# Kernel tuning notes

Measured on AMD Instinct MI355X. Metric: run time of the kernel, lower is better.

The kernel has to match this reference:

```python
import jax, jax.numpy as jnp
import numpy as np

H, P, N, D, T, MLPW, B = 64, 4, 16, 8, 64, 512, 2048
D_IN = 1 + H + P * H  # 321


def _linear_init(key, i, o):
    k1, k2 = jax.random.split(key)
    s = 1.0 / np.sqrt(i)
    W = jax.random.uniform(k1, (i, o), jnp.float32, -s, s)
    b = jax.random.uniform(k2, (o,), jnp.float32, -s, s)
    return W, b


def setup_inputs() -> dict:
    key = jax.random.key(0)
    ks = jax.random.split(key, 10)
    dims_f = [(D_IN, MLPW), (MLPW, MLPW), (MLPW, MLPW), (MLPW, H)]
    dims_g = [(D_IN, MLPW), (MLPW, MLPW), (MLPW, MLPW), (MLPW, H * N)]
    inp = {}
    for idx, (i, o) in enumerate(dims_f):
        W, b = _linear_init(ks[idx], i, o)
        inp[f"fW{idx}"], inp[f"fb{idx}"] = W, b
    for idx, (i, o) in enumerate(dims_g):
        W, b = _linear_init(ks[4 + idx], i, o)
        inp[f"gW{idx}"], inp[f"gb{idx}"] = W, b
    inp["rW"], inp["rb"] = _linear_init(ks[8], H, D)
    inp["ts"] = jnp.arange(T, dtype=jnp.float32)  # uniform grid, dt = 1
    inp["dbt"] = jax.random.normal(ks[9], (T - 1, B, N), jnp.float32)  # per-step randn noise
    inp["batch_size"] = B
    return inp


def _mlp(x, params):
    # Linear+ReLU stack, final Linear with tanh (tscale=1.0)
    for W, b in params[:-1]:
        x = jax.nn.relu(x @ W + b)
    W, b = params[-1]
    return jnp.tanh(x @ W + b)


def _forward(ts, dbt, fp, gp, rW, rb, batch_size):
    x0 = jnp.ones((batch_size, H), jnp.float32)  # fixed=True initial state
    dt = ts[1] - ts[0]  # dt_scale = 1
    hist = jnp.zeros((T, batch_size, H), jnp.float32).at[0].set(x0)
    curr_x, curr_t = x0, ts[0]
    xs = [x0]
    for k in range(T - 1):  # one integration step per output interval (uniform ts)
        # ortho rfft over the growing state history (length k+1); keep first P coeffs,
        # real part (matches torch complex -> .float() cast), zero-pad to P.
        coeffs = jnp.fft.rfft(hist[: k + 1], axis=0, norm="ortho")  # (F, B, H) complex
        c = jnp.real(coeffs[:P]).astype(jnp.float32)
        if c.shape[0] < P:
            c = jnp.concatenate(
                [c, jnp.zeros((P - c.shape[0], batch_size, H), jnp.float32)], axis=0
            )
        feats = jnp.transpose(c, (1, 0, 2)).reshape(batch_size, P * H)  # (B, P*H)
        tcol = jnp.broadcast_to(jnp.reshape(curr_t, (1, 1)), (batch_size, 1))
        tx = jnp.concatenate([tcol, curr_x, feats], axis=1)  # (B, 1+H+P*H)
        drift = _mlp(tx, fp)  # (B, H)
        diff = _mlp(tx, gp).reshape(batch_size, H, N)  # (B, H, N)
        curr_x = curr_x + drift * dt + jnp.einsum("bhn,bn->bh", diff, dbt[k])
        curr_t = jnp.minimum(curr_t + dt, ts[-1])
        hist = hist.at[k + 1].set(curr_x)
        xs.append(curr_x)  # linear_interp degenerates to curr_x on uniform grid
    xs = jnp.stack(xs, axis=1)  # (B, T, H)
    ys = xs @ rW + rb  # readout, (B, T, D)
    tse = jnp.broadcast_to(ts[None, :, None], (batch_size, T, 1))
    # linear_interpolation_coeffs is identity for NaN-free data
    return jnp.concatenate([tse, ys], axis=2)  # (B, T, 1+D)


def reference(fW0, fb0, fW1, fb1, fW2, fb2, fW3, fb3,
              gW0, gb0, gW1, gb1, gW2, gb2, gW3, gb3,
              rW, rb, ts, dbt, batch_size):
    fp = [(fW0, fb0), (fW1, fb1), (fW2, fb2), (fW3, fb3)]
    gp = [(gW0, gb0), (gW1, gb1), (gW2, gb2), (gW3, gb3)]
    return _forward(ts, dbt, fp, gp, rW, rb, batch_size)
```

## Files before the change

### kernel.cpp

```cpp
#include <hip/hip_runtime.h>
#include <math.h>

constexpr int kH   = 64;
constexpr int kP   = 4;
constexpr int kN   = 16;
constexpr int kD   = 8;
constexpr int kT   = 64;
constexpr int kWd  = 512;
constexpr int kB   = 2048;
constexpr int kDIN = 1 + kH + kP * kH;
constexpr int kKP  = 384;
constexpr int kBH  = kB * kH;

typedef __attribute__((ext_vector_type(8))) short short8;
typedef __attribute__((ext_vector_type(4))) float f32x4;
typedef __attribute__((ext_vector_type(4))) float float4v;

__device__ __forceinline__ short f2bf(float x) {
    union { float f; unsigned u; } v; v.f = x;
    unsigned r = (v.u + 0x7FFFu + ((v.u >> 16) & 1u)) >> 16;
    return (short)r;
}

__device__ __forceinline__ void gload16(const short* g, short* l) {
    __builtin_amdgcn_global_load_lds(
        (const __attribute__((address_space(1))) unsigned int*)g,
        (__attribute__((address_space(3))) unsigned int*)l, 16, 0, 0);
}

__global__ __launch_bounds__(256) void transpose_bf16(const float* __restrict__ W,
                                                      short* __restrict__ Wt,
                                                      int K, int N, int Kp, int Np) {
    int idx = blockIdx.x * 256 + threadIdx.x;
    if (idx >= Kp * Np) return;
    int n = idx / Kp, kk = idx % Kp;
    float v = (kk < K && n < N) ? W[(size_t)kk * N + n] : 0.f;
    Wt[idx] = f2bf(v);
}

__global__ __launch_bounds__(256) void prep_bias(const float* __restrict__ fb0,
                                                 const float* __restrict__ gb0,
                                                 float* __restrict__ b0c) {
    int i = blockIdx.x * 256 + threadIdx.x;
    if (i < 1024) b0c[i] = (i < kWd) ? fb0[i] : gb0[i - kWd];
}

__global__ __launch_bounds__(256) void init_k(float* __restrict__ hist,
                                              short* __restrict__ txh) {
    int idx = blockIdx.x * 256 + threadIdx.x;
    if (idx < kBH) hist[idx] = 1.0f;
    if (idx < kB * (kKP - kDIN)) {
        int b = idx / (kKP - kDIN), c = idx % (kKP - kDIN);
        txh[(size_t)b * kKP + kDIN + c] = 0;
    }
}

__global__ __launch_bounds__(256) void step_pre(float* __restrict__ hist,
                                                const float* __restrict__ drift,
                                                const float* __restrict__ xdelta,
                                                short* __restrict__ txh, int k) {
    const int L = k + 1;
    __shared__ float ctab[kT * kP];
    int tid = threadIdx.x;
    float invs = rsqrtf((float)L);
    for (int i = tid; i < L * kP; i += 256) {
        int j = i >> 2, p = i & 3;
        ctab[i] = cosf(6.283185307179586f * (float)(p * j) / (float)L) * invs;
    }
    __syncthreads();
    int idx = blockIdx.x * 256 + tid;
    int b = idx >> 6, h = idx & 63;
    float xk;
    if (k == 0) {
        xk = 1.0f;
    } else {
        xk = hist[(size_t)(k - 1) * kBH + idx] + drift[idx] + xdelta[idx];
        hist[(size_t)k * kBH + idx] = xk;
    }
    const float* hp = hist + (size_t)b * kH + h;
    float a0 = 0.f, a1 = 0.f, a2 = 0.f, a3 = 0.f;
    for (int j = 0; j < k; ++j) {
        float x = hp[(size_t)j * kBH];
        a0 += x * ctab[j * 4 + 0];
        a1 += x * ctab[j * 4 + 1];
        a2 += x * ctab[j * 4 + 2];
        a3 += x * ctab[j * 4 + 3];
    }
    a0 += xk * ctab[k * 4 + 0];
    a1 += xk * ctab[k * 4 + 1];
    a2 += xk * ctab[k * 4 + 2];
    a3 += xk * ctab[k * 4 + 3];
    if (L < 2) a1 = 0.f;
    if (L < 4) a2 = 0.f;
    if (L < 6) a3 = 0.f;
    short* th = txh + (size_t)b * kKP;
    th[1 + kH + 0 * kH + h] = f2bf(a0);
    th[1 + kH + 1 * kH + h] = f2bf(a1);
    th[1 + kH + 2 * kH + h] = f2bf(a2);
    th[1 + kH + 3 * kH + h] = f2bf(a3);
    th[1 + h] = f2bf(xk);
    if (h == 0) th[0] = f2bf((float)k);
}

struct MArg {
    const short* A;
    const short* Bt;
    const float* bias;
    short* Cb;
    int K, lda, ldc, Nw;
};

__global__ __launch_bounds__(512, 1) void gemm128(MArg f, MArg g, int ysplit) {
    const int y = blockIdx.y;
    MArg a;
    int n0;
    if (y < ysplit) { a = f; n0 = y * 64; }
    else            { a = g; n0 = (y - ysplit) * 64; }
    const int m0 = blockIdx.x * 128;

    __shared__ __align__(16) short sA[2][2][128 * 32];
    __shared__ __align__(16) short sB[2][2][64 * 32];

    const int tid = threadIdx.x;
    const int lane = tid & 63;
    const int w = tid >> 6;
    const int wm = (w & 3) * 32;
    const int wn = (w >> 2) * 32;

    const int sr = tid >> 2;
    const int s  = tid & 3;
    const int scol = (s ^ ((sr >> 1) & 3)) * 8;
    const int sdst = sr * 32 + s * 8;
    const bool doB = tid < 256;

    const short* gA = a.A  + (size_t)(m0 + sr) * a.lda + scol;
    const short* gB = a.Bt + (size_t)(n0 + sr) * a.K   + scol;

    const int nk = a.K >> 6;
    f32x4 acc[2][2] = {};

    gload16(gA,      &sA[0][0][sdst]);
    gload16(gA + 32, &sA[0][1][sdst]);
    if (doB) {
        gload16(gB,      &sB[0][0][sdst]);
        gload16(gB + 32, &sB[0][1][sdst]);
    }

    const int fr = lane & 15;
    const int kb = ((lane >> 4) ^ ((fr >> 1) & 3)) * 8;
    const int ra0 = (wm + fr) * 32 + kb, ra1 = (wm + 16 + fr) * 32 + kb;
    const int rb0 = (wn + fr) * 32 + kb, rb1 = (wn + 16 + fr) * 32 + kb;

    for (int kt = 0; kt < nk; ++kt) {
        __syncthreads();
        const int cur = kt & 1, nxt = cur ^ 1;
        if (kt + 1 < nk) {
            const int ko = (kt + 1) << 6;
            gload16(gA + ko,      &sA[nxt][0][sdst]);
            gload16(gA + ko + 32, &sA[nxt][1][sdst]);
            if (doB) {
                gload16(gB + ko,      &sB[nxt][0][sdst]);
                gload16(gB + ko + 32, &sB[nxt][1][sdst]);
            }
        }
#pragma unroll
        for (int ks = 0; ks < 2; ++ks) {
            short8 a0 = *(const short8*)&sA[cur][ks][ra0];
            short8 a1 = *(const short8*)&sA[cur][ks][ra1];
            short8 b0 = *(const short8*)&sB[cur][ks][rb0];
            short8 b1 = *(const short8*)&sB[cur][ks][rb1];
            acc[0][0] = __builtin_amdgcn_mfma_f32_16x16x32_bf16(a0, b0, acc[0][0], 0, 0, 0);
            acc[0][1] = __builtin_amdgcn_mfma_f32_16x16x32_bf16(a0, b1, acc[0][1], 0, 0, 0);
            acc[1][0] = __builtin_amdgcn_mfma_f32_16x16x32_bf16(a1, b0, acc[1][0], 0, 0, 0);
            acc[1][1] = __builtin_amdgcn_mfma_f32_16x16x32_bf16(a1, b1, acc[1][1], 0, 0, 0);
        }
    }

    const int rq = (lane >> 4) * 4;
#pragma unroll
    for (int jj = 0; jj < 2; ++jj) {
        int n = n0 + wn + jj * 16 + fr;
        if (n >= a.Nw) continue;
        float bv = a.bias[n];
#pragma unroll
        for (int i = 0; i < 2; ++i)
#pragma unroll
            for (int r = 0; r < 4; ++r) {
                int m = m0 + wm + i * 16 + rq + r;
                a.Cb[(size_t)m * a.ldc + n] = f2bf(fmaxf(acc[i][jj][r] + bv, 0.f));
            }
    }
}

__global__ __launch_bounds__(512, 1) void l4_kernel(const short* __restrict__ b1,
                                                    const short* __restrict__ fW3t,
                                                    const float* __restrict__ fb3,
                                                    const short* __restrict__ gW3t,
                                                    const float* __restrict__ gb3,
                                                    const float* __restrict__ dbt,
                                                    float* __restrict__ drift,
                                                    float* __restrict__ xdelta, int k) {
    const int y = blockIdx.y;
    const bool isF = (y == 0);
    const int nt = isF ? 0 : y - 1;
    const int n0 = nt * 64;
    const int m0 = blockIdx.x * 128;

    __shared__ __align__(16) short sA[2][2][128 * 32];
    __shared__ __align__(16) short sB[2][2][64 * 32];
    __shared__ float sdb[128 * 16];

    const int tid = threadIdx.x;
    const int lane = tid & 63;
    const int w = tid >> 6;
    const int wm = (w & 3) * 32;
    const int wn = (w >> 2) * 32;

    const short* A = b1 + (isF ? 0 : 512);
    const short* Bt = isF ? fW3t : gW3t + (size_t)n0 * 512;
    const float* bias = isF ? fb3 : gb3 + n0;
    const int K = 512;

    if (!isF)
        *(float4v*)&sdb[tid * 4] =
            ((const float4v*)(dbt + ((size_t)k * kB + m0) * kN))[tid];

    const int sr = tid >> 2;
    const int s  = tid & 3;
    const int scol = (s ^ ((sr >> 1) & 3)) * 8;
    const int sdst = sr * 32 + s * 8;
    const bool doB = tid < 256;

    const short* gA = A + (size_t)(m0 + sr) * 1024 + scol;
    const short* gB = Bt + (size_t)sr * K + scol;

    f32x4 acc[2][2] = {};
    gload16(gA,      &sA[0][0][sdst]);
    gload16(gA + 32, &sA[0][1][sdst]);
    if (doB) {
        gload16(gB,      &sB[0][0][sdst]);
        gload16(gB + 32, &sB[0][1][sdst]);
    }

    const int fr = lane & 15;
    const int kb = ((lane >> 4) ^ ((fr >> 1) & 3)) * 8;
    const int ra0 = (wm + fr) * 32 + kb, ra1 = (wm + 16 + fr) * 32 + kb;
    const int rb0 = (wn + fr) * 32 + kb, rb1 = (wn + 16 + fr) * 32 + kb;

    for (int kt = 0; kt < 8; ++kt) {
        __syncthreads();
        const int cur = kt & 1, nxt = cur ^ 1;
        if (kt + 1 < 8) {
            const int ko = (kt + 1) << 6;
            gload16(gA + ko,      &sA[nxt][0][sdst]);
            gload16(gA + ko + 32, &sA[nxt][1][sdst]);
            if (doB) {
                gload16(gB + ko,      &sB[nxt][0][sdst]);
                gload16(gB + ko + 32, &sB[nxt][1][sdst]);
            }
        }
#pragma unroll
        for (int ks = 0; ks < 2; ++ks) {
            short8 a0 = *(const short8*)&sA[cur][ks][ra0];
            short8 a1 = *(const short8*)&sA[cur][ks][ra1];
            short8 b0 = *(const short8*)&sB[cur][ks][rb0];
            short8 b1 = *(const short8*)&sB[cur][ks][rb1];
            acc[0][0] = __builtin_amdgcn_mfma_f32_16x16x32_bf16(a0, b0, acc[0][0], 0, 0, 0);
            acc[0][1] = __builtin_amdgcn_mfma_f32_16x16x32_bf16(a0, b1, acc[0][1], 0, 0, 0);
            acc[1][0] = __builtin_amdgcn_mfma_f32_16x16x32_bf16(a1, b0, acc[1][0], 0, 0, 0);
            acc[1][1] = __builtin_amdgcn_mfma_f32_16x16x32_bf16(a1, b1, acc[1][1], 0, 0, 0);
        }
    }

    const int rq = (lane >> 4) * 4;
    if (isF) {
#pragma unroll
        for (int jj = 0; jj < 2; ++jj) {
            int n = wn + jj * 16 + fr;
            float bv = bias[n];
#pragma unroll
            for (int i = 0; i < 2; ++i)
#pragma unroll
                for (int r = 0; r < 4; ++r) {
                    int m = m0 + wm + i * 16 + rq + r;
                    drift[(size_t)m * kH + n] = tanhf(acc[i][jj][r] + bv);
                }
        }
    } else {
#pragma unroll
        for (int jj = 0; jj < 2; ++jj) {
            int n = wn + jj * 16 + fr;
            float bv = bias[n];
            int h = (n0 + wn + jj * 16) >> 4;
#pragma unroll
            for (int i = 0; i < 2; ++i)
#pragma unroll
                for (int r = 0; r < 4; ++r) {
                    int mr = wm + i * 16 + rq + r;
                    float v = tanhf(acc[i][jj][r] + bv);
                    float p = v * sdb[mr * 16 + fr];
                    p += __shfl_xor(p, 1);
                    p += __shfl_xor(p, 2);
                    p += __shfl_xor(p, 4);
                    p += __shfl_xor(p, 8);
                    if (fr == 0)
                        xdelta[(size_t)(m0 + mr) * kH + h] = p;
                }
        }
    }
}

__global__ __launch_bounds__(256) void update_k(float* __restrict__ hist,
                                                const float* __restrict__ drift,
                                                const float* __restrict__ xdelta, int k) {
    int idx = blockIdx.x * 256 + threadIdx.x;
    hist[(size_t)(k + 1) * kBH + idx] =
        hist[(size_t)k * kBH + idx] + drift[idx] + xdelta[idx];
}

__global__ __launch_bounds__(256) void readout_k(const float* __restrict__ hist,
                                                 const float* __restrict__ rW,
                                                 const float* __restrict__ rb,
                                                 const float* __restrict__ ts,
                                                 float* __restrict__ out) {
    __shared__ float sW[kH * kD];
    __shared__ float sb[kD];
    __shared__ float sts[kT];
    int tid = threadIdx.x;
    sW[tid] = rW[tid];
    sW[tid + 256] = rW[tid + 256];
    if (tid < kD) sb[tid] = rb[tid];
    if (tid < kT) sts[tid] = ts[tid];
    __syncthreads();
    int idx = blockIdx.x * 256 + tid;
    int t = idx & (kT - 1), b = idx >> 6;
    const float* xr = hist + (size_t)t * kBH + (size_t)b * kH;
    float acc[kD];
#pragma unroll
    for (int d = 0; d < kD; ++d) acc[d] = sb[d];
    for (int h = 0; h < kH; ++h) {
        float x = xr[h];
#pragma unroll
        for (int d = 0; d < kD; ++d) acc[d] += x * sW[h * kD + d];
    }
    float* o = out + (size_t)((size_t)b * kT + t) * (1 + kD);
    o[0] = sts[t];
#pragma unroll
    for (int d = 0; d < kD; ++d) o[1 + d] = acc[d];
}

extern "C" void kernel_launch(void* const* d_in, const int* in_sizes, int n_in,
                              void* d_out, int out_size, void* d_ws, size_t ws_size,
                              hipStream_t stream) {
    const float* fW0 = (const float*)d_in[0];  const float* fb0 = (const float*)d_in[1];
    const float* fW1 = (const float*)d_in[2];  const float* fb1 = (const float*)d_in[3];
    const float* fW2 = (const float*)d_in[4];  const float* fb2 = (const float*)d_in[5];
    const float* fW3 = (const float*)d_in[6];  const float* fb3 = (const float*)d_in[7];
    const float* gW0 = (const float*)d_in[8];  const float* gb0 = (const float*)d_in[9];
    const float* gW1 = (const float*)d_in[10]; const float* gb1 = (const float*)d_in[11];
    const float* gW2 = (const float*)d_in[12]; const float* gb2 = (const float*)d_in[13];
    const float* gW3 = (const float*)d_in[14]; const float* gb3 = (const float*)d_in[15];
    const float* rW  = (const float*)d_in[16]; const float* rb  = (const float*)d_in[17];
    const float* ts  = (const float*)d_in[18]; const float* dbt = (const float*)d_in[19];
    float* out = (float*)d_out;

    char* p = (char*)d_ws;
    float* hist   = (float*)p;  p += (size_t)kT * kBH * 4;
    float* drift  = (float*)p;  p += (size_t)kBH * 4;
    float* xdelta = (float*)p;  p += (size_t)kBH * 4;
    float* b0c    = (float*)p;  p += 1024 * 4;
    short* txh    = (short*)p;  p += (size_t)kB * kKP * 2;
    short* b1h    = (short*)p;  p += (size_t)kB * 1024 * 2;
    short* b2h    = (short*)p;  p += (size_t)kB * 1024 * 2;
    short* W0t    = (short*)p;  p += (size_t)1024 * kKP * 2;
    short* fW1t   = (short*)p;  p += (size_t)512 * 512 * 2;
    short* gW1t   = (short*)p;  p += (size_t)512 * 512 * 2;
    short* fW2t   = (short*)p;  p += (size_t)512 * 512 * 2;
    short* gW2t   = (short*)p;  p += (size_t)512 * 512 * 2;
    short* fW3t   = (short*)p;  p += (size_t)64 * 512 * 2;
    short* gW3t   = (short*)p;  p += (size_t)1024 * 512 * 2;

    auto tgrid = [](int n) { return dim3((n + 255) / 256); };
    transpose_bf16<<<tgrid(kKP * 512), 256, 0, stream>>>(fW0, W0t, kDIN, 512, kKP, 512);
    transpose_bf16<<<tgrid(kKP * 512), 256, 0, stream>>>(gW0, W0t + (size_t)512 * kKP, kDIN, 512, kKP, 512);
    transpose_bf16<<<tgrid(512 * 512), 256, 0, stream>>>(fW1, fW1t, 512, 512, 512, 512);
    transpose_bf16<<<tgrid(512 * 512), 256, 0, stream>>>(gW1, gW1t, 512, 512, 512, 512);
    transpose_bf16<<<tgrid(512 * 512), 256, 0, stream>>>(fW2, fW2t, 512, 512, 512, 512);
    transpose_bf16<<<tgrid(512 * 512), 256, 0, stream>>>(gW2, gW2t, 512, 512, 512, 512);
    transpose_bf16<<<tgrid(512 * 64), 256, 0, stream>>>(fW3, fW3t, 512, 64, 512, 64);
    transpose_bf16<<<tgrid(512 * 1024), 256, 0, stream>>>(gW3, gW3t, 512, 1024, 512, 1024);
    prep_bias<<<dim3(4), 256, 0, stream>>>(fb0, gb0, b0c);
    init_k<<<dim3(kBH / 256), 256, 0, stream>>>(hist, txh);

    for (int k = 0; k < kT - 1; ++k) {
        step_pre<<<dim3(kBH / 256), 256, 0, stream>>>(hist, drift, xdelta, txh, k);

        MArg l1{txh, W0t, b0c, b1h, kKP, kKP, 1024, 1024};
        gemm128<<<dim3(16, 16), 512, 0, stream>>>(l1, l1, 16);

        MArg f2{b1h, fW1t, fb1, b2h, 512, 1024, 1024, 512};
        MArg g2{b1h + 512, gW1t, gb1, b2h + 512, 512, 1024, 1024, 512};
        gemm128<<<dim3(16, 16), 512, 0, stream>>>(f2, g2, 8);

        MArg f3{b2h, fW2t, fb2, b1h, 512, 1024, 1024, 512};
        MArg g3{b2h + 512, gW2t, gb2, b1h + 512, 512, 1024, 1024, 512};
        gemm128<<<dim3(16, 16), 512, 0, stream>>>(f3, g3, 8);

        l4_kernel<<<dim3(16, 17), 512, 0, stream>>>(b1h, fW3t, fb3, gW3t, gb3,
                                                    dbt, drift, xdelta, k);
    }

    update_k<<<dim3(kBH / 256), 256, 0, stream>>>(hist, drift, xdelta, kT - 2);
    readout_k<<<dim3(kB * kT / 256), 256, 0, stream>>>(hist, rW, rb, ts, out);
}
```

Measured before the change: 2.608 ms.

## Fuse DFT feature prep into layer-1 GEMM and shrink GEMM tiles to 64x64

Removes the separate step_pre kernel and the txh buffer. Each layer-1 GEMM block now computes its own state update and rfft features straight into swizzled shared memory, reading a new bf16 copy of the history. All GEMMs move from 128x64 tiles with 512 threads to 64x64 tiles with 256 threads, plus a block-index swizzle, so the grid has twice as many blocks. The aim is to save one launch and a global round-trip per step and to fill the GPU better. In exchange, the history reduction is repeated by all 16 column tiles, and the bf16 history lowers the precision of the DFT features.

```diff
diff --git a/kernel.cpp b/kernel.cpp
--- a/kernel.cpp
+++ b/kernel.cpp
@@ -21,6 +21,10 @@
     unsigned r = (v.u + 0x7FFFu + ((v.u >> 16) & 1u)) >> 16;
     return (short)r;
 }
+__device__ __forceinline__ float bf2f(short h) {
+    union { unsigned u; float f; } v; v.u = ((unsigned)(unsigned short)h) << 16;
+    return v.f;
+}
 
 __device__ __forceinline__ void gload16(const short* g, short* l) {
     __builtin_amdgcn_global_load_lds(
@@ -45,93 +49,155 @@
     if (i < 1024) b0c[i] = (i < kWd) ? fb0[i] : gb0[i - kWd];
 }
 
-__global__ __launch_bounds__(256) void init_k(float* __restrict__ hist,
-                                              short* __restrict__ txh) {
-    int idx = blockIdx.x * 256 + threadIdx.x;
-    if (idx < kBH) hist[idx] = 1.0f;
-    if (idx < kB * (kKP - kDIN)) {
-        int b = idx / (kKP - kDIN), c = idx % (kKP - kDIN);
-        txh[(size_t)b * kKP + kDIN + c] = 0;
-    }
-}
-
-__global__ __launch_bounds__(256) void step_pre(float* __restrict__ hist,
-                                                const float* __restrict__ drift,
-                                                const float* __restrict__ xdelta,
-                                                short* __restrict__ txh, int k) {
+__global__ __launch_bounds__(256, 2) void l1_fused(
+    float* __restrict__ hist, short* __restrict__ histb,
+    const float* __restrict__ drift, const float* __restrict__ xdelta,
+    const short* __restrict__ W0t, const float* __restrict__ b0c,
+    short* __restrict__ b1h, int k) {
+    __shared__ __align__(16) short sTX[12 * 64 * 32];
+    __shared__ __align__(16) short sB[2][2][64 * 32];
+    __shared__ float ctab[kT * kP];
+
+    const int bid = blockIdx.x;
+    const int c = bid & 7, t = bid >> 3;
+    const int mt = c + 8 * (t & 3);
+    const int nt = t >> 2;
+    const int m0 = mt * 64, n0 = nt * 64;
+    const int tid = threadIdx.x;
     const int L = k + 1;
-    __shared__ float ctab[kT * kP];
-    int tid = threadIdx.x;
-    float invs = rsqrtf((float)L);
-    for (int i = tid; i < L * kP; i += 256) {
+
+    for (int i = tid; i < L * 4; i += 256) {
         int j = i >> 2, p = i & 3;
-        ctab[i] = cosf(6.283185307179586f * (float)(p * j) / (float)L) * invs;
+        ctab[i] = cosf(6.283185307179586f * (float)(p * j) / (float)L) *
+                  rsqrtf((float)L);
     }
     __syncthreads();
-    int idx = blockIdx.x * 256 + tid;
-    int b = idx >> 6, h = idx & 63;
-    float xk;
-    if (k == 0) {
-        xk = 1.0f;
-    } else {
-        xk = hist[(size_t)(k - 1) * kBH + idx] + drift[idx] + xdelta[idx];
-        hist[(size_t)k * kBH + idx] = xk;
-    }
-    const float* hp = hist + (size_t)b * kH + h;
-    float a0 = 0.f, a1 = 0.f, a2 = 0.f, a3 = 0.f;
-    for (int j = 0; j < k; ++j) {
-        float x = hp[(size_t)j * kBH];
-        a0 += x * ctab[j * 4 + 0];
-        a1 += x * ctab[j * 4 + 1];
-        a2 += x * ctab[j * 4 + 2];
-        a3 += x * ctab[j * 4 + 3];
-    }
-    a0 += xk * ctab[k * 4 + 0];
-    a1 += xk * ctab[k * 4 + 1];
-    a2 += xk * ctab[k * 4 + 2];
-    a3 += xk * ctab[k * 4 + 3];
-    if (L < 2) a1 = 0.f;
-    if (L < 4) a2 = 0.f;
-    if (L < 6) a3 = 0.f;
-    short* th = txh + (size_t)b * kKP;
-    th[1 + kH + 0 * kH + h] = f2bf(a0);
-    th[1 + kH + 1 * kH + h] = f2bf(a1);
-    th[1 + kH + 2 * kH + h] = f2bf(a2);
-    th[1 + kH + 3 * kH + h] = f2bf(a3);
-    th[1 + h] = f2bf(xk);
-    if (h == 0) th[0] = f2bf((float)k);
+
+    auto stx = [&](int row, int col, float v) {
+        int p = col >> 5, s = (col >> 3) & 3;
+        sTX[p * 2048 + row * 32 + (((s ^ ((row >> 1) & 3))) << 3) + (col & 7)] =
+            f2bf(v);
+    };
+
+    for (int i = tid; i < 64 * 64; i += 256) {
+        int row = i >> 6, h = i & 63;
+        int bg = m0 + row;
+        float xk;
+        if (k == 0) {
+            xk = 1.0f;
+        } else {
+            xk = hist[(size_t)(k - 1) * kBH + bg * 64 + h] +
+                 drift[bg * 64 + h] + xdelta[bg * 64 + h];
+        }
+        if (nt == 0) {
+            hist[(size_t)k * kBH + bg * 64 + h] = xk;
+            histb[(size_t)k * kBH + bg * 64 + h] = f2bf(xk);
+        }
+        float a0 = 0.f, a1 = 0.f, a2 = 0.f, a3 = 0.f;
+        const short* hb = histb + (size_t)bg * 64 + h;
+        for (int j = 0; j < k; ++j) {
+            float x = bf2f(hb[(size_t)j * kBH]);
+            a0 += x * ctab[j * 4 + 0];
+            a1 += x * ctab[j * 4 + 1];
+            a2 += x * ctab[j * 4 + 2];
+            a3 += x * ctab[j * 4 + 3];
+        }
+        a0 += xk * ctab[k * 4 + 0];
+        a1 += xk * ctab[k * 4 + 1];
+        a2 += xk * ctab[k * 4 + 2];
+        a3 += xk * ctab[k * 4 + 3];
+        if (L < 2) a1 = 0.f;
+        if (L < 4) a2 = 0.f;
+        if (L < 6) a3 = 0.f;
+        stx(row, 1 + h, xk);
+        stx(row, 65 + 0 * 64 + h, a0);
+        stx(row, 65 + 1 * 64 + h, a1);
+        stx(row, 65 + 2 * 64 + h, a2);
+        stx(row, 65 + 3 * 64 + h, a3);
+        if (h == 0) stx(row, 0, (float)k);
+        if (h < 63) stx(row, 321 + h, 0.f);
+    }
+
+    const int lane = tid & 63, w = tid >> 6;
+    const int wm = (w & 1) * 32, wn = (w >> 1) * 32;
+    const int sr = tid >> 2, s = tid & 3;
+    const int scol = (s ^ ((sr >> 1) & 3)) * 8;
+    const int sdst = sr * 32 + s * 8;
+    const short* gB = W0t + (size_t)(n0 + sr) * kKP + scol;
+
+    f32x4 acc[2][2] = {};
+    gload16(gB,      &sB[0][0][sdst]);
+    gload16(gB + 32, &sB[0][1][sdst]);
+
+    const int fr = lane & 15;
+    const int kb = ((lane >> 4) ^ ((fr >> 1) & 3)) * 8;
+
+    for (int kt = 0; kt < 6; ++kt) {
+        __syncthreads();
+        const int cur = kt & 1, nxt = cur ^ 1;
+        if (kt + 1 < 6) {
+            const int ko = (kt + 1) << 6;
+            gload16(gB + ko,      &sB[nxt][0][sdst]);
+            gload16(gB + ko + 32, &sB[nxt][1][sdst]);
+        }
+#pragma unroll
+        for (int ks = 0; ks < 2; ++ks) {
+            const short* pa = &sTX[(kt * 2 + ks) * 2048];
+            short8 a0 = *(const short8*)&pa[(wm + fr) * 32 + kb];
+            short8 a1 = *(const short8*)&pa[(wm + 16 + fr) * 32 + kb];
+            short8 b0 = *(const short8*)&sB[cur][ks][(wn + fr) * 32 + kb];
+            short8 b1 = *(const short8*)&sB[cur][ks][(wn + 16 + fr) * 32 + kb];
+            acc[0][0] = __builtin_amdgcn_mfma_f32_16x16x32_bf16(a0, b0, acc[0][0], 0, 0, 0);
+            acc[0][1] = __builtin_amdgcn_mfma_f32_16x16x32_bf16(a0, b1, acc[0][1], 0, 0, 0);
+            acc[1][0] = __builtin_amdgcn_mfma_f32_16x16x32_bf16(a1, b0, acc[1][0], 0, 0, 0);
+            acc[1][1] = __builtin_amdgcn_mfma_f32_16x16x32_bf16(a1, b1, acc[1][1], 0, 0, 0);
+        }
+    }
+
+    const int rq = (lane >> 4) * 4;
+#pragma unroll
+    for (int j = 0; j < 2; ++j) {
+        int n = n0 + wn + j * 16 + fr;
+        float bv = b0c[n];
+#pragma unroll
+        for (int i = 0; i < 2; ++i)
+#pragma unroll
+            for (int r = 0; r < 4; ++r) {
+                int m = m0 + wm + i * 16 + rq + r;
+                b1h[(size_t)m * 1024 + n] = f2bf(fmaxf(acc[i][j][r] + bv, 0.f));
+            }
+    }
 }
 
 struct MArg {
-    const short* A;
-    const short* Bt;
-    const float* bias;
-    short* Cb;
-    int K, lda, ldc, Nw;
+    const short* A; const short* Bt; const float* bias;
+    short* Cb; int K, lda, ldc, Nw;
 };
 
-__global__ __launch_bounds__(512, 1) void gemm128(MArg f, MArg g, int ysplit) {
-    const int y = blockIdx.y;
+__global__ __launch_bounds__(256, 2) void gemm_mfma(MArg f, MArg g, int ysplit) {
+    const int bid = blockIdx.x;
+    const int c = bid & 7, t = bid >> 3;
+    const int mt = c + 8 * (t & 3);
+    const int nt = t >> 2;
     MArg a;
     int n0;
-    if (y < ysplit) { a = f; n0 = y * 64; }
-    else            { a = g; n0 = (y - ysplit) * 64; }
-    const int m0 = blockIdx.x * 128;
-
-    __shared__ __align__(16) short sA[2][2][128 * 32];
+    if (nt < ysplit) { a = f; n0 = nt * 64; }
+    else             { a = g; n0 = (nt - ysplit) * 64; }
+    const int m0 = mt * 64;
+
+    __shared__ __align__(16) short sA[2][2][64 * 32];
     __shared__ __align__(16) short sB[2][2][64 * 32];
 
     const int tid = threadIdx.x;
     const int lane = tid & 63;
     const int w = tid >> 6;
-    const int wm = (w & 3) * 32;
-    const int wn = (w >> 2) * 32;
+    const int wm = (w & 1) * 32;
+    const int wn = (w >> 1) * 32;
 
     const int sr = tid >> 2;
     const int s  = tid & 3;
     const int scol = (s ^ ((sr >> 1) & 3)) * 8;
     const int sdst = sr * 32 + s * 8;
-    const bool doB = tid < 256;
 
     const short* gA = a.A  + (size_t)(m0 + sr) * a.lda + scol;
     const short* gB = a.Bt + (size_t)(n0 + sr) * a.K   + scol;
@@ -141,10 +207,8 @@
 
     gload16(gA,      &sA[0][0][sdst]);
     gload16(gA + 32, &sA[0][1][sdst]);
-    if (doB) {
-        gload16(gB,      &sB[0][0][sdst]);
-        gload16(gB + 32, &sB[0][1][sdst]);
-    }
+    gload16(gB,      &sB[0][0][sdst]);
+    gload16(gB + 32, &sB[0][1][sdst]);
 
     const int fr = lane & 15;
     const int kb = ((lane >> 4) ^ ((fr >> 1) & 3)) * 8;
@@ -158,10 +222,8 @@
             const int ko = (kt + 1) << 6;
             gload16(gA + ko,      &sA[nxt][0][sdst]);
             gload16(gA + ko + 32, &sA[nxt][1][sdst]);
-            if (doB) {
-                gload16(gB + ko,      &sB[nxt][0][sdst]);
-                gload16(gB + ko + 32, &sB[nxt][1][sdst]);
-            }
+            gload16(gB + ko,      &sB[nxt][0][sdst]);
+            gload16(gB + ko + 32, &sB[nxt][1][sdst]);
         }
 #pragma unroll
         for (int ks = 0; ks < 2; ++ks) {
@@ -178,8 +240,8 @@
 
     const int rq = (lane >> 4) * 4;
 #pragma unroll
-    for (int jj = 0; jj < 2; ++jj) {
-        int n = n0 + wn + jj * 16 + fr;
+    for (int j = 0; j < 2; ++j) {
+        int n = n0 + wn + j * 16 + fr;
         if (n >= a.Nw) continue;
         float bv = a.bias[n];
 #pragma unroll
@@ -187,60 +249,53 @@
 #pragma unroll
             for (int r = 0; r < 4; ++r) {
                 int m = m0 + wm + i * 16 + rq + r;
-                a.Cb[(size_t)m * a.ldc + n] = f2bf(fmaxf(acc[i][jj][r] + bv, 0.f));
+                a.Cb[(size_t)m * a.ldc + n] = f2bf(fmaxf(acc[i][j][r] + bv, 0.f));
             }
     }
 }
 
-__global__ __launch_bounds__(512, 1) void l4_kernel(const short* __restrict__ b1,
-                                                    const short* __restrict__ fW3t,
-                                                    const float* __restrict__ fb3,
-                                                    const short* __restrict__ gW3t,
-                                                    const float* __restrict__ gb3,
-                                                    const float* __restrict__ dbt,
-                                                    float* __restrict__ drift,
-                                                    float* __restrict__ xdelta, int k) {
+__global__ __launch_bounds__(256, 2) void l4_kernel(
+    const short* __restrict__ b1, const short* __restrict__ fW3t,
+    const float* __restrict__ fb3, const short* __restrict__ gW3t,
+    const float* __restrict__ gb3, const float* __restrict__ dbt,
+    float* __restrict__ drift, float* __restrict__ xdelta, int k) {
     const int y = blockIdx.y;
     const bool isF = (y == 0);
     const int nt = isF ? 0 : y - 1;
     const int n0 = nt * 64;
-    const int m0 = blockIdx.x * 128;
-
-    __shared__ __align__(16) short sA[2][2][128 * 32];
+    const int m0 = blockIdx.x * 64;
+
+    __shared__ __align__(16) short sA[2][2][64 * 32];
     __shared__ __align__(16) short sB[2][2][64 * 32];
-    __shared__ float sdb[128 * 16];
+    __shared__ float sdb[64 * 16];
 
     const int tid = threadIdx.x;
     const int lane = tid & 63;
     const int w = tid >> 6;
-    const int wm = (w & 3) * 32;
-    const int wn = (w >> 2) * 32;
+    const int wm = (w & 1) * 32;
+    const int wn = (w >> 1) * 32;
+
+    if (!isF)
+        *(float4v*)&sdb[tid * 4] =
+            *(const float4v*)(dbt + ((size_t)k * kB + m0) * kN + tid * 4);
 
     const short* A = b1 + (isF ? 0 : 512);
     const short* Bt = isF ? fW3t : gW3t + (size_t)n0 * 512;
-    const float* bias = isF ? fb3 : gb3 + n0;
-    const int K = 512;
-
-    if (!isF)
-        *(float4v*)&sdb[tid * 4] =
-            ((const float4v*)(dbt + ((size_t)k * kB + m0) * kN))[tid];
+    const float* bias = isF ? fb3 : gb3;
 
     const int sr = tid >> 2;
     const int s  = tid & 3;
     const int scol = (s ^ ((sr >> 1) & 3)) * 8;
     const int sdst = sr * 32 + s * 8;
-    const bool doB = tid < 256;
 
     const short* gA = A + (size_t)(m0 + sr) * 1024 + scol;
-    const short* gB = Bt + (size_t)sr * K + scol;
+    const short* gB = Bt + (size_t)sr * 512 + scol;
 
     f32x4 acc[2][2] = {};
     gload16(gA,      &sA[0][0][sdst]);
     gload16(gA + 32, &sA[0][1][sdst]);
-    if (doB) {
-        gload16(gB,      &sB[0][0][sdst]);
-        gload16(gB + 32, &sB[0][1][sdst]);
-    }
+    gload16(gB,      &sB[0][0][sdst]);
+    gload16(gB + 32, &sB[0][1][sdst]);
 
     const int fr = lane & 15;
     const int kb = ((lane >> 4) ^ ((fr >> 1) & 3)) * 8;
@@ -254,10 +309,8 @@
             const int ko = (kt + 1) << 6;
             gload16(gA + ko,      &sA[nxt][0][sdst]);
             gload16(gA + ko + 32, &sA[nxt][1][sdst]);
-            if (doB) {
-                gload16(gB + ko,      &sB[nxt][0][sdst]);
-                gload16(gB + ko + 32, &sB[nxt][1][sdst]);
-            }
+            gload16(gB + ko,      &sB[nxt][0][sdst]);
+            gload16(gB + ko + 32, &sB[nxt][1][sdst]);
         }
 #pragma unroll
         for (int ks = 0; ks < 2; ++ks) {
@@ -275,36 +328,36 @@
     const int rq = (lane >> 4) * 4;
     if (isF) {
 #pragma unroll
-        for (int jj = 0; jj < 2; ++jj) {
-            int n = wn + jj * 16 + fr;
+        for (int j = 0; j < 2; ++j) {
+            int n = wn + j * 16 + fr;
             float bv = bias[n];
 #pragma unroll
             for (int i = 0; i < 2; ++i)
 #pragma unroll
                 for (int r = 0; r < 4; ++r) {
                     int m = m0 + wm + i * 16 + rq + r;
-                    drift[(size_t)m * kH + n] = tanhf(acc[i][jj][r] + bv);
+                    drift[(size_t)m * kH + n] = tanhf(acc[i][j][r] + bv);
                 }
         }
     } else {
 #pragma unroll
-        for (int jj = 0; jj < 2; ++jj) {
-            int n = wn + jj * 16 + fr;
-            float bv = bias[n];
-            int h = (n0 + wn + jj * 16) >> 4;
+        for (int j = 0; j < 2; ++j) {
+            int ng = n0 + wn + j * 16 + fr;
+            float bv = bias[ng];
+            int h = (n0 + wn + j * 16) >> 4;
 #pragma unroll
             for (int i = 0; i < 2; ++i)
 #pragma unroll
                 for (int r = 0; r < 4; ++r) {
-                    int mr = wm + i * 16 + rq + r;
-                    float v = tanhf(acc[i][jj][r] + bv);
-                    float p = v * sdb[mr * 16 + fr];
+                    int row = wm + i * 16 + rq + r;
+                    float v = tanhf(acc[i][j][r] + bv);
+                    float p = v * sdb[row * 16 + fr];
                     p += __shfl_xor(p, 1);
                     p += __shfl_xor(p, 2);
                     p += __shfl_xor(p, 4);
                     p += __shfl_xor(p, 8);
                     if (fr == 0)
-                        xdelta[(size_t)(m0 + mr) * kH + h] = p;
+                        xdelta[(size_t)(m0 + row) * kH + h] = p;
                 }
         }
     }
@@ -366,10 +419,10 @@
 
     char* p = (char*)d_ws;
     float* hist   = (float*)p;  p += (size_t)kT * kBH * 4;
+    short* histb  = (short*)p;  p += (size_t)(kT - 1) * kBH * 2;
     float* drift  = (float*)p;  p += (size_t)kBH * 4;
     float* xdelta = (float*)p;  p += (size_t)kBH * 4;
     float* b0c    = (float*)p;  p += 1024 * 4;
-    short* txh    = (short*)p;  p += (size_t)kB * kKP * 2;
     short* b1h    = (short*)p;  p += (size_t)kB * 1024 * 2;
     short* b2h    = (short*)p;  p += (size_t)kB * 1024 * 2;
     short* W0t    = (short*)p;  p += (size_t)1024 * kKP * 2;
@@ -390,23 +443,20 @@
     transpose_bf16<<<tgrid(512 * 64), 256, 0, stream>>>(fW3, fW3t, 512, 64, 512, 64);
     transpose_bf16<<<tgrid(512 * 1024), 256, 0, stream>>>(gW3, gW3t, 512, 1024, 512, 1024);
     prep_bias<<<dim3(4), 256, 0, stream>>>(fb0, gb0, b0c);
-    init_k<<<dim3(kBH / 256), 256, 0, stream>>>(hist, txh);
 
     for (int k = 0; k < kT - 1; ++k) {
-        step_pre<<<dim3(kBH / 256), 256, 0, stream>>>(hist, drift, xdelta, txh, k);
-
-        MArg l1{txh, W0t, b0c, b1h, kKP, kKP, 1024, 1024};
-        gemm128<<<dim3(16, 16), 512, 0, stream>>>(l1, l1, 16);
+        l1_fused<<<dim3(512), 256, 0, stream>>>(hist, histb, drift, xdelta,
+                                                W0t, b0c, b1h, k);
 
         MArg f2{b1h, fW1t, fb1, b2h, 512, 1024, 1024, 512};
         MArg g2{b1h + 512, gW1t, gb1, b2h + 512, 512, 1024, 1024, 512};
-        gemm128<<<dim3(16, 16), 512, 0, stream>>>(f2, g2, 8);
+        gemm_mfma<<<dim3(32 * 16), 256, 0, stream>>>(f2, g2, 8);
 
         MArg f3{b2h, fW2t, fb2, b1h, 512, 1024, 1024, 512};
         MArg g3{b2h + 512, gW2t, gb2, b1h + 512, 512, 1024, 1024, 512};
-        gemm128<<<dim3(16, 16), 512, 0, stream>>>(f3, g3, 8);
-
-        l4_kernel<<<dim3(16, 17), 512, 0, stream>>>(b1h, fW3t, fb3, gW3t, gb3,
+        gemm_mfma<<<dim3(32 * 16), 256, 0, stream>>>(f3, g3, 8);
+
+        l4_kernel<<<dim3(32, 17), 256, 0, stream>>>(b1h, fW3t, fb3, gW3t, gb3,
                                                     dbt, drift, xdelta, k);
     }
 
```

New measurement: 4.920 ms. 1.89x slower.
